# Optimization experiments

Hardware: AMD Instinct MI355X
Metric: run time of the kernel (lower is better)

The kernel has to match this reference:

```python
import jax, jax.numpy as jnp
import numpy as np

N_ENT = 50000
N_REL = 500
DIM = 128
B = 1024
N_EDGES = 800000
BN_EPS = 1e-5


def setup_inputs() -> dict:
    key = jax.random.key(0)
    ks = jax.random.split(key, 12)
    return {
        "E_emb": jax.random.normal(ks[0], (N_ENT, DIM), jnp.float32),
        "R_emb": jax.random.normal(ks[1], (N_REL, DIM), jnp.float32),
        "W1": jax.random.normal(ks[2], (DIM, DIM), jnp.float32) / np.sqrt(DIM),
        "b1": jax.random.normal(ks[3], (DIM,), jnp.float32) * 0.01,
        "W2": jax.random.normal(ks[4], (DIM, DIM), jnp.float32) / np.sqrt(DIM),
        "b2": jax.random.normal(ks[5], (DIM,), jnp.float32) * 0.01,
        "W": jax.random.normal(ks[6], (DIM, DIM), jnp.float32) / np.sqrt(DIM),
        "adj_vals": jax.random.uniform(ks[7], (N_EDGES,), jnp.float32) / 16.0,
        "bn0_gamma": jnp.ones((DIM,), jnp.float32),
        "bn0_beta": jnp.zeros((DIM,), jnp.float32),
        "bn1_gamma": jnp.ones((DIM,), jnp.float32),
        "bn1_beta": jnp.zeros((DIM,), jnp.float32),
        "batch_head": jax.random.randint(ks[8], (B,), 0, N_ENT, jnp.int32),
        "batch_rel": jax.random.randint(ks[9], (B,), 0, N_REL, jnp.int32),
        "init_ind": jnp.arange(N_ENT, dtype=jnp.int32),
        "adj_rows": jax.random.randint(ks[10], (N_EDGES,), 0, N_ENT, jnp.int32),
        "adj_cols": jax.random.randint(ks[11], (N_EDGES,), 0, N_ENT, jnp.int32),
    }


def _bn_eval(x, gamma, beta):
    # BatchNorm1d in eval mode with running_mean=0, running_var=1
    return x * (gamma / jnp.sqrt(1.0 + BN_EPS)) + beta


def _spmm(rows, cols, vals, dense):
    # out[i] = sum_{e: rows[e]==i} vals[e] * dense[cols[e]]
    gathered = dense[cols] * vals[:, None]  # [E, DIM]
    return jax.ops.segment_sum(gathered, rows, num_segments=N_ENT)


def reference(E_emb, R_emb, W1, b1, W2, b2, W, adj_vals,
              bn0_gamma, bn0_beta, bn1_gamma, bn1_beta,
              batch_head, batch_rel, init_ind, adj_rows, adj_cols):
    init_emb = E_emb[init_ind]                                  # [N, D]
    h = jax.nn.relu(_spmm(adj_rows, adj_cols, adj_vals, init_emb @ W1) + b1)
    h = jax.nn.relu(_spmm(adj_rows, adj_cols, adj_vals, h @ W2) + b2)
    final_emb = init_emb + h                                    # shortcut connection
    x = _bn_eval(final_emb[batch_head], bn0_gamma, bn0_beta)    # [B, D]
    r = R_emb[batch_rel]                                        # [B, D]
    W_mat = r @ W                                               # mat_vec_mul: [B, D]
    vm = _bn_eval(x * W_mat, bn1_gamma, bn1_beta)               # [B, D]
    dot = vm @ final_emb.T                                      # [B, N]
    return jax.nn.sigmoid(dot)
```

## Files before the change

kernel.cpp:

```cpp
#include <hip/hip_runtime.h>

#define N_ENT   50000
#define N_EDGES 800000
#define DIM     128
#define BATCH   1024

typedef _Float16 half_t;
typedef __attribute__((ext_vector_type(8))) _Float16 half8;
typedef __attribute__((ext_vector_type(2))) _Float16 half2v;
typedef __attribute__((ext_vector_type(4))) float float4v;
typedef __attribute__((ext_vector_type(2))) float float2v;

__global__ void k_hist(const int* __restrict__ rows, int* __restrict__ deg){
    int e = blockIdx.x*256 + threadIdx.x;
    if(e < N_EDGES) atomicAdd(&deg[rows[e]], 1);
}

__global__ void k_scan(const int* __restrict__ deg, int* __restrict__ row_start){
    __shared__ int part[1024];
    const int CH = 49;
    int t = threadIdx.x;
    int base = t*CH;
    int s = 0;
    for(int i=0;i<CH;i++){ int idx=base+i; if(idx<N_ENT) s += deg[idx]; }
    part[t]=s; __syncthreads();
    for(int off=1; off<1024; off<<=1){
        int v = part[t];
        int add = (t>=off)? part[t-off] : 0;
        __syncthreads();
        part[t] = v+add;
        __syncthreads();
    }
    int run = part[t]-s;
    for(int i=0;i<CH;i++){
        int idx=base+i;
        if(idx<=N_ENT){
            row_start[idx]=run;
            if(idx<N_ENT) run += deg[idx];
        }
    }
}

__global__ void k_scatter(const int* __restrict__ rows, const int* __restrict__ cols,
                          const float* __restrict__ vals, const int* __restrict__ row_start,
                          int* __restrict__ cursor, int* __restrict__ csr_col,
                          float* __restrict__ csr_val){
    int e = blockIdx.x*256 + threadIdx.x;
    if(e >= N_EDGES) return;
    int r = rows[e];
    int pos = row_start[r] + atomicAdd(&cursor[r], 1);
    csr_col[pos] = cols[e];
    csr_val[pos] = vals[e];
}

__global__ void k_prep(const float* __restrict__ W1, const float* __restrict__ W2,
                       half_t* __restrict__ W1T_hi, half_t* __restrict__ W1T_lo,
                       half_t* __restrict__ W2T_hi, half_t* __restrict__ W2T_lo){
    int i = blockIdx.x*256 + threadIdx.x;
    const float* src = (i < 16384) ? W1 : W2;
    half_t* dh = (i < 16384) ? W1T_hi : W2T_hi;
    half_t* dl = (i < 16384) ? W1T_lo : W2T_lo;
    int j = i & 16383;
    int d = j >> 7, c = j & 127;
    float f = src[j];
    half_t h = (half_t)f;
    dh[c*DIM + d] = h;
    dl[c*DIM + d] = (half_t)(f - (float)h);
}

__global__ __launch_bounds__(256) void k_mm1(const float* __restrict__ E,
                                             const int* __restrict__ init_ind,
                                             const half_t* __restrict__ WT_hi,
                                             const half_t* __restrict__ WT_lo,
                                             half_t* __restrict__ t_out){
    int wave = threadIdx.x >> 6, lane = threadIdx.x & 63;
    int mt = blockIdx.x*4 + wave;
    if(mt >= 3125) return;
    int m = lane & 15, q = lane >> 4;
    int row = init_ind[mt*16 + m];
    const float* ap = E + (long)row*DIM + q*8;
    float4v acc[8];
    #pragma unroll
    for(int i=0;i<8;i++) acc[i] = (float4v){0.f,0.f,0.f,0.f};
    #pragma unroll
    for(int ks=0; ks<4; ks++){
        float4v u0 = *(const float4v*)(ap + ks*32);
        float4v u1 = *(const float4v*)(ap + ks*32 + 4);
        half8 ah, al;
        #pragma unroll
        for(int j=0;j<8;j++){
            float fv = (j<4) ? u0[j] : u1[j-4];
            half_t h = (half_t)fv;
            ah[j] = h;
            al[j] = (half_t)(fv - (float)h);
        }
        #pragma unroll
        for(int nt=0; nt<8; nt++){
            half8 bh = *(const half8*)(WT_hi + (nt*16 + m)*DIM + ks*32 + q*8);
            half8 bl = *(const half8*)(WT_lo + (nt*16 + m)*DIM + ks*32 + q*8);
            acc[nt] = __builtin_amdgcn_mfma_f32_16x16x32_f16(ah, bh, acc[nt], 0,0,0);
            acc[nt] = __builtin_amdgcn_mfma_f32_16x16x32_f16(ah, bl, acc[nt], 0,0,0);
            acc[nt] = __builtin_amdgcn_mfma_f32_16x16x32_f16(al, bh, acc[nt], 0,0,0);
        }
    }
    #pragma unroll
    for(int nt=0; nt<8; nt++)
        #pragma unroll
        for(int r=0;r<4;r++)
            t_out[(mt*16 + q*4 + r)*DIM + nt*16 + m] = (half_t)acc[nt][r];
}

__global__ __launch_bounds__(256) void k_mm2(const half_t* __restrict__ h_hi,
                                             const half_t* __restrict__ h_lo,
                                             const half_t* __restrict__ WT_hi,
                                             const half_t* __restrict__ WT_lo,
                                             half_t* __restrict__ t_out){
    int wave = threadIdx.x >> 6, lane = threadIdx.x & 63;
    int mt = blockIdx.x*4 + wave;
    if(mt >= 3125) return;
    int m = lane & 15, q = lane >> 4;
    int row = mt*16 + m;
    const half_t* ah_p = h_hi + (long)row*DIM + q*8;
    const half_t* al_p = h_lo + (long)row*DIM + q*8;
    float4v acc[8];
    #pragma unroll
    for(int i=0;i<8;i++) acc[i] = (float4v){0.f,0.f,0.f,0.f};
    #pragma unroll
    for(int ks=0; ks<4; ks++){
        half8 ah = *(const half8*)(ah_p + ks*32);
        half8 al = *(const half8*)(al_p + ks*32);
        #pragma unroll
        for(int nt=0; nt<8; nt++){
            half8 bh = *(const half8*)(WT_hi + (nt*16 + m)*DIM + ks*32 + q*8);
            half8 bl = *(const half8*)(WT_lo + (nt*16 + m)*DIM + ks*32 + q*8);
            acc[nt] = __builtin_amdgcn_mfma_f32_16x16x32_f16(ah, bh, acc[nt], 0,0,0);
            acc[nt] = __builtin_amdgcn_mfma_f32_16x16x32_f16(ah, bl, acc[nt], 0,0,0);
            acc[nt] = __builtin_amdgcn_mfma_f32_16x16x32_f16(al, bh, acc[nt], 0,0,0);
        }
    }
    #pragma unroll
    for(int nt=0; nt<8; nt++)
        #pragma unroll
        for(int r=0;r<4;r++)
            t_out[(mt*16 + q*4 + r)*DIM + nt*16 + m] = (half_t)acc[nt][r];
}

__global__ __launch_bounds__(256) void k_spmm1(const half_t* __restrict__ t,
        const int* __restrict__ row_start, const int* __restrict__ csr_col,
        const float* __restrict__ csr_val, const float* __restrict__ b1,
        half_t* __restrict__ h_hi, half_t* __restrict__ h_lo){
    int wave = threadIdx.x>>6, lane = threadIdx.x&63;
    int i = blockIdx.x*4 + wave;
    if(i >= N_ENT) return;
    int e0 = __builtin_amdgcn_readfirstlane(row_start[i]);
    int e1 = __builtin_amdgcn_readfirstlane(row_start[i+1]);
    const half2v* tp = (const half2v*)t;
    float a0=0.f, a1=0.f;
    int e = e0;
    for(; e+4<=e1; e+=4){
        int c0=csr_col[e], c1=csr_col[e+1], c2=csr_col[e+2], c3=csr_col[e+3];
        float v0=csr_val[e], v1=csr_val[e+1], v2=csr_val[e+2], v3=csr_val[e+3];
        half2v p0=tp[c0*64+lane], p1=tp[c1*64+lane], p2=tp[c2*64+lane], p3=tp[c3*64+lane];
        a0 += v0*(float)p0[0]; a1 += v0*(float)p0[1];
        a0 += v1*(float)p1[0]; a1 += v1*(float)p1[1];
        a0 += v2*(float)p2[0]; a1 += v2*(float)p2[1];
        a0 += v3*(float)p3[0]; a1 += v3*(float)p3[1];
    }
    for(; e<e1; e++){
        int c = csr_col[e]; float v = csr_val[e];
        half2v p = tp[c*64+lane];
        a0 += v*(float)p[0]; a1 += v*(float)p[1];
    }
    float2v bb = *(const float2v*)(b1 + lane*2);
    float r0 = fmaxf(a0 + bb[0], 0.f);
    float r1 = fmaxf(a1 + bb[1], 0.f);
    half_t h0=(half_t)r0, h1=(half_t)r1;
    half2v hi = {h0, h1};
    half2v lo = {(half_t)(r0-(float)h0), (half_t)(r1-(float)h1)};
    *(half2v*)(h_hi + (long)i*DIM + lane*2) = hi;
    *(half2v*)(h_lo + (long)i*DIM + lane*2) = lo;
}

__global__ __launch_bounds__(256) void k_spmm2(const half_t* __restrict__ t,
        const int* __restrict__ row_start, const int* __restrict__ csr_col,
        const float* __restrict__ csr_val, const float* __restrict__ b2_,
        const float* __restrict__ E, const int* __restrict__ init_ind,
        half_t* __restrict__ fe_hi, half_t* __restrict__ fe_lo){
    int wave = threadIdx.x>>6, lane = threadIdx.x&63;
    int i = blockIdx.x*4 + wave;
    if(i >= N_ENT) return;
    int e0 = __builtin_amdgcn_readfirstlane(row_start[i]);
    int e1 = __builtin_amdgcn_readfirstlane(row_start[i+1]);
    const half2v* tp = (const half2v*)t;
    float a0=0.f, a1=0.f;
    int e = e0;
    for(; e+4<=e1; e+=4){
        int c0=csr_col[e], c1=csr_col[e+1], c2=csr_col[e+2], c3=csr_col[e+3];
        float v0=csr_val[e], v1=csr_val[e+1], v2=csr_val[e+2], v3=csr_val[e+3];
        half2v p0=tp[c0*64+lane], p1=tp[c1*64+lane], p2=tp[c2*64+lane], p3=tp[c3*64+lane];
        a0 += v0*(float)p0[0]; a1 += v0*(float)p0[1];
        a0 += v1*(float)p1[0]; a1 += v1*(float)p1[1];
        a0 += v2*(float)p2[0]; a1 += v2*(float)p2[1];
        a0 += v3*(float)p3[0]; a1 += v3*(float)p3[1];
    }
    for(; e<e1; e++){
        int c = csr_col[e]; float v = csr_val[e];
        half2v p = tp[c*64+lane];
        a0 += v*(float)p[0]; a1 += v*(float)p[1];
    }
    int erow = init_ind[i];
    float2v ev = *(const float2v*)(E + (long)erow*DIM + lane*2);
    float2v bb = *(const float2v*)(b2_ + lane*2);
    float f0 = ev[0] + fmaxf(a0 + bb[0], 0.f);
    float f1 = ev[1] + fmaxf(a1 + bb[1], 0.f);
    half_t h0=(half_t)f0, h1=(half_t)f1;
    half2v hi = {h0, h1};
    half2v lo = {(half_t)(f0-(float)h0), (half_t)(f1-(float)h1)};
    *(half2v*)(fe_hi + (long)i*DIM + lane*2) = hi;
    *(half2v*)(fe_lo + (long)i*DIM + lane*2) = lo;
}

__global__ __launch_bounds__(128) void k_vm(const float* __restrict__ R_emb,
        const float* __restrict__ W, const int* __restrict__ head,
        const int* __restrict__ rel, const half_t* __restrict__ fe_hi,
        const half_t* __restrict__ fe_lo, const float* __restrict__ g0v,
        const float* __restrict__ be0, const float* __restrict__ g1v,
        const float* __restrict__ be1, half_t* __restrict__ vm_hi,
        half_t* __restrict__ vm_lo){
    int b = blockIdx.x; int j = threadIdx.x;
    __shared__ float rs[DIM];
    int rid = rel[b], hid = head[b];
    rs[j] = R_emb[rid*DIM + j];
    __syncthreads();
    float acc = 0.f;
    #pragma unroll 8
    for(int d=0; d<DIM; d++) acc += rs[d] * W[d*DIM + j];
    const float inv = rsqrtf(1.f + 1e-5f);
    float fe = (float)fe_hi[(long)hid*DIM+j] + (float)fe_lo[(long)hid*DIM+j];
    float x  = fe * (g0v[j] * inv) + be0[j];
    float vmv = (x * acc) * (g1v[j] * inv) + be1[j];
    half_t hi = (half_t)vmv;
    vm_hi[b*DIM+j] = hi;
    vm_lo[b*DIM+j] = (half_t)(vmv - (float)hi);
}

__global__ __launch_bounds__(256) void k_big(const half_t* __restrict__ vm_hi,
        const half_t* __restrict__ vm_lo, const half_t* __restrict__ fe_h,
        float* __restrict__ out){
    __shared__ float sl[16*260];
    int wave = threadIdx.x>>6, lane = threadIdx.x&63;
    int m = lane&15, q = lane>>4;
    int b0 = blockIdx.y * 64;
    int n0 = blockIdx.x * 256 + wave*64;
    float4v acc[4][4];
    #pragma unroll
    for(int a=0;a<4;a++)
        #pragma unroll
        for(int b=0;b<4;b++) acc[a][b] = (float4v){0.f,0.f,0.f,0.f};
    #pragma unroll
    for(int ks=0; ks<4; ks++){
        half8 B[4], Ah[4], Al[4];
        #pragma unroll
        for(int nt=0;nt<4;nt++){
            int nr = n0 + nt*16 + m;
            if(nr > N_ENT-1) nr = N_ENT-1;
            B[nt] = *(const half8*)(fe_h + (long)nr*DIM + ks*32 + q*8);
        }
        #pragma unroll
        for(int mt=0;mt<4;mt++){
            long ao = (long)(b0 + mt*16 + m)*DIM + ks*32 + q*8;
            Ah[mt] = *(const half8*)(vm_hi + ao);
            Al[mt] = *(const half8*)(vm_lo + ao);
        }
        #pragma unroll
        for(int mt=0;mt<4;mt++)
            #pragma unroll
            for(int nt=0;nt<4;nt++){
                acc[mt][nt] = __builtin_amdgcn_mfma_f32_16x16x32_f16(Ah[mt], B[nt], acc[mt][nt], 0,0,0);
                acc[mt][nt] = __builtin_amdgcn_mfma_f32_16x16x32_f16(Al[mt], B[nt], acc[mt][nt], 0,0,0);
            }
    }
    int gcol = blockIdx.x*256 + lane*4;
    #pragma unroll
    for(int mt=0; mt<4; mt++){
        if(mt) __syncthreads();
        #pragma unroll
        for(int nt=0;nt<4;nt++)
            #pragma unroll
            for(int r=0;r<4;r++){
                float d = acc[mt][nt][r];
                float s = __fdividef(1.f, 1.f + __expf(-d));
                sl[(q*4+r)*260 + wave*64 + nt*16 + m] = s;
            }
        __syncthreads();
        if(gcol < N_ENT){
            #pragma unroll
            for(int k=0;k<4;k++){
                int lr = wave*4 + k;
                float4v vv = *(const float4v*)&sl[lr*260 + lane*4];
                long off = (long)(b0 + mt*16 + lr)*N_ENT + gcol;
                __builtin_nontemporal_store(vv, (float4v*)(out + off));
            }
        }
    }
}

extern "C" void kernel_launch(void* const* d_in, const int* in_sizes, int n_in,
                              void* d_out, int out_size, void* d_ws, size_t ws_size,
                              hipStream_t stream) {
    const float* E     = (const float*)d_in[0];
    const float* R_emb = (const float*)d_in[1];
    const float* W1    = (const float*)d_in[2];
    const float* b1    = (const float*)d_in[3];
    const float* W2    = (const float*)d_in[4];
    const float* b2_   = (const float*)d_in[5];
    const float* W     = (const float*)d_in[6];
    const float* vals  = (const float*)d_in[7];
    const float* g0v   = (const float*)d_in[8];
    const float* be0   = (const float*)d_in[9];
    const float* g1v   = (const float*)d_in[10];
    const float* be1   = (const float*)d_in[11];
    const int* head    = (const int*)d_in[12];
    const int* rel     = (const int*)d_in[13];
    const int* init_ind= (const int*)d_in[14];
    const int* rows    = (const int*)d_in[15];
    const int* cols    = (const int*)d_in[16];
    float* out = (float*)d_out;

    char* w = (char*)d_ws;
    int*    deg       = (int*)   (w + 0);
    int*    cursor    = (int*)   (w + 200000);
    int*    row_start = (int*)   (w + 400000);
    int*    csr_col   = (int*)   (w + 600064);
    float*  csr_val   = (float*) (w + 3800064);
    half_t* W1T_hi    = (half_t*)(w + 7000064);
    half_t* W1T_lo    = (half_t*)(w + 7032832);
    half_t* W2T_hi    = (half_t*)(w + 7065600);
    half_t* W2T_lo    = (half_t*)(w + 7098368);
    half_t* t         = (half_t*)(w + 7131136);
    half_t* h_hi      = (half_t*)(w + 19931136);
    half_t* h_lo      = (half_t*)(w + 32731136);
    half_t* fe_hi     = (half_t*)(w + 45531136);
    half_t* fe_lo     = (half_t*)(w + 58331136);
    half_t* vm_hi     = (half_t*)(w + 71131136);
    half_t* vm_lo     = (half_t*)(w + 71393280);

    hipMemsetAsync(deg, 0, 2*N_ENT*sizeof(int), stream);
    k_hist    <<<3125, 256, 0, stream>>>(rows, deg);
    k_scan    <<<1, 1024, 0, stream>>>(deg, row_start);
    k_scatter <<<3125, 256, 0, stream>>>(rows, cols, vals, row_start, cursor, csr_col, csr_val);
    k_prep    <<<128, 256, 0, stream>>>(W1, W2, W1T_hi, W1T_lo, W2T_hi, W2T_lo);
    k_mm1     <<<782, 256, 0, stream>>>(E, init_ind, W1T_hi, W1T_lo, t);
    k_spmm1   <<<12500, 256, 0, stream>>>(t, row_start, csr_col, csr_val, b1, h_hi, h_lo);
    k_mm2     <<<782, 256, 0, stream>>>(h_hi, h_lo, W2T_hi, W2T_lo, t);
    k_spmm2   <<<12500, 256, 0, stream>>>(t, row_start, csr_col, csr_val, b2_, E, init_ind, fe_hi, fe_lo);
    k_vm      <<<BATCH, 128, 0, stream>>>(R_emb, W, head, rel, fe_hi, fe_lo, g0v, be0, g1v, be1, vm_hi, vm_lo);
    k_big     <<<dim3(196, 16), 256, 0, stream>>>(vm_hi, vm_lo, fe_hi, out);
}
```

Measured before the change: 634.8 us.

## Fuse preprocessing kernels, fuse spmm1 with mm2, interleave CSR col/val pairs

Combines the histogram, weight transpose/split and the relation-times-W projection into one launch, and runs the scan alongside the first dense GEMM in a single launch. The first SpMM now writes its 16-row tile into shared memory and immediately multiplies it by W2, so the h_hi/h_lo intermediates no longer go through global memory. CSR columns and values are stored as interleaved int pairs, and the gather loops are unrolled to 8 edges. This removes launches and intermediate traffic. In exchange the fused SpMM-GEMM has fewer waves per row tile and a barrier before the MFMA stage, and the combined scan block may serialize behind the GEMM blocks.

```diff
diff --git a/kernel.cpp b/kernel.cpp
--- a/kernel.cpp
+++ b/kernel.cpp
@@ -1,6 +1,7 @@
 #include <hip/hip_runtime.h>
 
 #define N_ENT   50000
+#define N_REL   500
 #define N_EDGES 800000
 #define DIM     128
 #define BATCH   1024
@@ -10,71 +11,77 @@
 typedef __attribute__((ext_vector_type(2))) _Float16 half2v;
 typedef __attribute__((ext_vector_type(4))) float float4v;
 typedef __attribute__((ext_vector_type(2))) float float2v;
-
-__global__ void k_hist(const int* __restrict__ rows, int* __restrict__ deg){
-    int e = blockIdx.x*256 + threadIdx.x;
-    if(e < N_EDGES) atomicAdd(&deg[rows[e]], 1);
-}
-
-__global__ void k_scan(const int* __restrict__ deg, int* __restrict__ row_start){
-    __shared__ int part[1024];
-    const int CH = 49;
-    int t = threadIdx.x;
-    int base = t*CH;
-    int s = 0;
-    for(int i=0;i<CH;i++){ int idx=base+i; if(idx<N_ENT) s += deg[idx]; }
-    part[t]=s; __syncthreads();
-    for(int off=1; off<1024; off<<=1){
-        int v = part[t];
-        int add = (t>=off)? part[t-off] : 0;
+typedef __attribute__((ext_vector_type(2))) int int2v;
+
+__global__ __launch_bounds__(256) void k_pre(
+        const int* __restrict__ rows, int* __restrict__ deg,
+        const float* __restrict__ W1, const float* __restrict__ W2,
+        half_t* __restrict__ W1T_hi, half_t* __restrict__ W1T_lo,
+        half_t* __restrict__ W2T_hi, half_t* __restrict__ W2T_lo,
+        const float* __restrict__ R_emb, const float* __restrict__ W,
+        const int* __restrict__ rel, float* __restrict__ Wr){
+    int blk = blockIdx.x;
+    if(blk < 3125){
+        int e = blk*256 + threadIdx.x;
+        if(e < N_EDGES) atomicAdd(&deg[rows[e]], 1);
+    } else if(blk < 3253){
+        int i = (blk-3125)*256 + threadIdx.x;
+        const float* src = (i < 16384) ? W1 : W2;
+        half_t* dh = (i < 16384) ? W1T_hi : W2T_hi;
+        half_t* dl = (i < 16384) ? W1T_lo : W2T_lo;
+        int j = i & 16383;
+        int d = j >> 7, c = j & 127;
+        float f = src[j];
+        half_t h = (half_t)f;
+        dh[c*DIM + d] = h;
+        dl[c*DIM + d] = (half_t)(f - (float)h);
+    } else {
+        __shared__ float rs[2][DIM];
+        int half_id = threadIdx.x >> 7;
+        int bb = (blk-3253)*2 + half_id;
+        int j = threadIdx.x & 127;
+        int rid = rel[bb];
+        rs[half_id][j] = R_emb[rid*DIM + j];
         __syncthreads();
-        part[t] = v+add;
-        __syncthreads();
-    }
-    int run = part[t]-s;
-    for(int i=0;i<CH;i++){
-        int idx=base+i;
-        if(idx<=N_ENT){
-            row_start[idx]=run;
-            if(idx<N_ENT) run += deg[idx];
-        }
-    }
-}
-
-__global__ void k_scatter(const int* __restrict__ rows, const int* __restrict__ cols,
-                          const float* __restrict__ vals, const int* __restrict__ row_start,
-                          int* __restrict__ cursor, int* __restrict__ csr_col,
-                          float* __restrict__ csr_val){
-    int e = blockIdx.x*256 + threadIdx.x;
-    if(e >= N_EDGES) return;
-    int r = rows[e];
-    int pos = row_start[r] + atomicAdd(&cursor[r], 1);
-    csr_col[pos] = cols[e];
-    csr_val[pos] = vals[e];
-}
-
-__global__ void k_prep(const float* __restrict__ W1, const float* __restrict__ W2,
-                       half_t* __restrict__ W1T_hi, half_t* __restrict__ W1T_lo,
-                       half_t* __restrict__ W2T_hi, half_t* __restrict__ W2T_lo){
-    int i = blockIdx.x*256 + threadIdx.x;
-    const float* src = (i < 16384) ? W1 : W2;
-    half_t* dh = (i < 16384) ? W1T_hi : W2T_hi;
-    half_t* dl = (i < 16384) ? W1T_lo : W2T_lo;
-    int j = i & 16383;
-    int d = j >> 7, c = j & 127;
-    float f = src[j];
-    half_t h = (half_t)f;
-    dh[c*DIM + d] = h;
-    dl[c*DIM + d] = (half_t)(f - (float)h);
-}
-
-__global__ __launch_bounds__(256) void k_mm1(const float* __restrict__ E,
-                                             const int* __restrict__ init_ind,
-                                             const half_t* __restrict__ WT_hi,
-                                             const half_t* __restrict__ WT_lo,
-                                             half_t* __restrict__ t_out){
+        float acc = 0.f;
+        #pragma unroll 8
+        for(int d=0; d<DIM; d++) acc += rs[half_id][d] * W[d*DIM + j];
+        Wr[bb*DIM + j] = acc;
+    }
+}
+
+__global__ __launch_bounds__(1024) void k_scan_mm1(
+        const int* __restrict__ deg, int* __restrict__ row_start,
+        const float* __restrict__ E, const int* __restrict__ init_ind,
+        const half_t* __restrict__ WT_hi, const half_t* __restrict__ WT_lo,
+        half_t* __restrict__ t_out){
+    if(blockIdx.x == 0){
+        __shared__ int part[1024];
+        const int CH = 49;
+        int t = threadIdx.x;
+        int base = t*CH;
+        int s = 0;
+        for(int i=0;i<CH;i++){ int idx=base+i; if(idx<N_ENT) s += deg[idx]; }
+        part[t]=s; __syncthreads();
+        for(int off=1; off<1024; off<<=1){
+            int v = part[t];
+            int add = (t>=off)? part[t-off] : 0;
+            __syncthreads();
+            part[t] = v+add;
+            __syncthreads();
+        }
+        int run = part[t]-s;
+        for(int i=0;i<CH;i++){
+            int idx=base+i;
+            if(idx<=N_ENT){
+                row_start[idx]=run;
+                if(idx<N_ENT) run += deg[idx];
+            }
+        }
+        return;
+    }
     int wave = threadIdx.x >> 6, lane = threadIdx.x & 63;
-    int mt = blockIdx.x*4 + wave;
+    int mt = (blockIdx.x-1)*16 + wave;
     if(mt >= 3125) return;
     int m = lane & 15, q = lane >> 4;
     int row = init_ind[mt*16 + m];
@@ -110,81 +117,107 @@
             t_out[(mt*16 + q*4 + r)*DIM + nt*16 + m] = (half_t)acc[nt][r];
 }
 
-__global__ __launch_bounds__(256) void k_mm2(const half_t* __restrict__ h_hi,
-                                             const half_t* __restrict__ h_lo,
-                                             const half_t* __restrict__ WT_hi,
-                                             const half_t* __restrict__ WT_lo,
-                                             half_t* __restrict__ t_out){
-    int wave = threadIdx.x >> 6, lane = threadIdx.x & 63;
-    int mt = blockIdx.x*4 + wave;
-    if(mt >= 3125) return;
+__global__ __launch_bounds__(256) void k_scatter(const int* __restrict__ rows,
+        const int* __restrict__ cols, const float* __restrict__ vals,
+        const int* __restrict__ row_start, int* __restrict__ cursor,
+        int2v* __restrict__ csr){
+    int e = blockIdx.x*256 + threadIdx.x;
+    if(e >= N_EDGES) return;
+    int r = rows[e];
+    int pos = row_start[r] + atomicAdd(&cursor[r], 1);
+    int2v p;
+    p[0] = cols[e];
+    p[1] = __float_as_int(vals[e]);
+    csr[pos] = p;
+}
+
+__global__ __launch_bounds__(256) void k_sp1mm2(
+        const half_t* __restrict__ t, const int* __restrict__ row_start,
+        const int2v* __restrict__ csr, const float* __restrict__ b1,
+        const half_t* __restrict__ WT_hi, const half_t* __restrict__ WT_lo,
+        half_t* __restrict__ t2){
+    __shared__ half_t hh[16][136];
+    __shared__ half_t hl[16][136];
+    int wave = threadIdx.x>>6, lane = threadIdx.x&63;
+    int mt = blockIdx.x;
+    const half2v* tp = (const half2v*)t;
+    float2v bb = *(const float2v*)(b1 + lane*2);
+    for(int rr=0; rr<4; rr++){
+        int i = mt*16 + wave*4 + rr;
+        int e0 = __builtin_amdgcn_readfirstlane(row_start[i]);
+        int e1 = __builtin_amdgcn_readfirstlane(row_start[i+1]);
+        float a0=0.f, a1=0.f;
+        int e = e0;
+        for(; e+8<=e1; e+=8){
+            int2v p0=csr[e],   p1=csr[e+1], p2=csr[e+2], p3=csr[e+3];
+            int2v p4=csr[e+4], p5=csr[e+5], p6=csr[e+6], p7=csr[e+7];
+            half2v g0=tp[p0[0]*64+lane], g1=tp[p1[0]*64+lane], g2=tp[p2[0]*64+lane], g3=tp[p3[0]*64+lane];
+            half2v g4=tp[p4[0]*64+lane], g5=tp[p5[0]*64+lane], g6=tp[p6[0]*64+lane], g7=tp[p7[0]*64+lane];
+            float v0=__int_as_float(p0[1]), v1=__int_as_float(p1[1]), v2=__int_as_float(p2[1]), v3=__int_as_float(p3[1]);
+            float v4=__int_as_float(p4[1]), v5=__int_as_float(p5[1]), v6=__int_as_float(p6[1]), v7=__int_as_float(p7[1]);
+            a0 += v0*(float)g0[0]; a1 += v0*(float)g0[1];
+            a0 += v1*(float)g1[0]; a1 += v1*(float)g1[1];
+            a0 += v2*(float)g2[0]; a1 += v2*(float)g2[1];
+            a0 += v3*(float)g3[0]; a1 += v3*(float)g3[1];
+            a0 += v4*(float)g4[0]; a1 += v4*(float)g4[1];
+            a0 += v5*(float)g5[0]; a1 += v5*(float)g5[1];
+            a0 += v6*(float)g6[0]; a1 += v6*(float)g6[1];
+            a0 += v7*(float)g7[0]; a1 += v7*(float)g7[1];
+        }
+        for(; e+4<=e1; e+=4){
+            int2v p0=csr[e], p1=csr[e+1], p2=csr[e+2], p3=csr[e+3];
+            half2v g0=tp[p0[0]*64+lane], g1=tp[p1[0]*64+lane], g2=tp[p2[0]*64+lane], g3=tp[p3[0]*64+lane];
+            float v0=__int_as_float(p0[1]), v1=__int_as_float(p1[1]), v2=__int_as_float(p2[1]), v3=__int_as_float(p3[1]);
+            a0 += v0*(float)g0[0]; a1 += v0*(float)g0[1];
+            a0 += v1*(float)g1[0]; a1 += v1*(float)g1[1];
+            a0 += v2*(float)g2[0]; a1 += v2*(float)g2[1];
+            a0 += v3*(float)g3[0]; a1 += v3*(float)g3[1];
+        }
+        for(; e<e1; e++){
+            int2v p = csr[e];
+            half2v g = tp[p[0]*64+lane];
+            float v = __int_as_float(p[1]);
+            a0 += v*(float)g[0]; a1 += v*(float)g[1];
+        }
+        float r0 = fmaxf(a0 + bb[0], 0.f);
+        float r1 = fmaxf(a1 + bb[1], 0.f);
+        half_t h0=(half_t)r0, h1=(half_t)r1;
+        int row = wave*4 + rr;
+        *(half2v*)&hh[row][lane*2] = (half2v){h0, h1};
+        *(half2v*)&hl[row][lane*2] = (half2v){(half_t)(r0-(float)h0), (half_t)(r1-(float)h1)};
+    }
+    __syncthreads();
     int m = lane & 15, q = lane >> 4;
-    int row = mt*16 + m;
-    const half_t* ah_p = h_hi + (long)row*DIM + q*8;
-    const half_t* al_p = h_lo + (long)row*DIM + q*8;
-    float4v acc[8];
-    #pragma unroll
-    for(int i=0;i<8;i++) acc[i] = (float4v){0.f,0.f,0.f,0.f};
+    float4v acc[2];
+    acc[0] = (float4v){0.f,0.f,0.f,0.f};
+    acc[1] = (float4v){0.f,0.f,0.f,0.f};
     #pragma unroll
     for(int ks=0; ks<4; ks++){
-        half8 ah = *(const half8*)(ah_p + ks*32);
-        half8 al = *(const half8*)(al_p + ks*32);
-        #pragma unroll
-        for(int nt=0; nt<8; nt++){
+        half8 ah = *(const half8*)&hh[m][ks*32 + q*8];
+        half8 al = *(const half8*)&hl[m][ks*32 + q*8];
+        #pragma unroll
+        for(int n=0; n<2; n++){
+            int nt = wave*2 + n;
             half8 bh = *(const half8*)(WT_hi + (nt*16 + m)*DIM + ks*32 + q*8);
             half8 bl = *(const half8*)(WT_lo + (nt*16 + m)*DIM + ks*32 + q*8);
-            acc[nt] = __builtin_amdgcn_mfma_f32_16x16x32_f16(ah, bh, acc[nt], 0,0,0);
-            acc[nt] = __builtin_amdgcn_mfma_f32_16x16x32_f16(ah, bl, acc[nt], 0,0,0);
-            acc[nt] = __builtin_amdgcn_mfma_f32_16x16x32_f16(al, bh, acc[nt], 0,0,0);
-        }
-    }
-    #pragma unroll
-    for(int nt=0; nt<8; nt++)
+            acc[n] = __builtin_amdgcn_mfma_f32_16x16x32_f16(ah, bh, acc[n], 0,0,0);
+            acc[n] = __builtin_amdgcn_mfma_f32_16x16x32_f16(ah, bl, acc[n], 0,0,0);
+            acc[n] = __builtin_amdgcn_mfma_f32_16x16x32_f16(al, bh, acc[n], 0,0,0);
+        }
+    }
+    #pragma unroll
+    for(int n=0; n<2; n++){
+        int nt = wave*2 + n;
         #pragma unroll
         for(int r=0;r<4;r++)
-            t_out[(mt*16 + q*4 + r)*DIM + nt*16 + m] = (half_t)acc[nt][r];
-}
-
-__global__ __launch_bounds__(256) void k_spmm1(const half_t* __restrict__ t,
-        const int* __restrict__ row_start, const int* __restrict__ csr_col,
-        const float* __restrict__ csr_val, const float* __restrict__ b1,
-        half_t* __restrict__ h_hi, half_t* __restrict__ h_lo){
-    int wave = threadIdx.x>>6, lane = threadIdx.x&63;
-    int i = blockIdx.x*4 + wave;
-    if(i >= N_ENT) return;
-    int e0 = __builtin_amdgcn_readfirstlane(row_start[i]);
-    int e1 = __builtin_amdgcn_readfirstlane(row_start[i+1]);
-    const half2v* tp = (const half2v*)t;
-    float a0=0.f, a1=0.f;
-    int e = e0;
-    for(; e+4<=e1; e+=4){
-        int c0=csr_col[e], c1=csr_col[e+1], c2=csr_col[e+2], c3=csr_col[e+3];
-        float v0=csr_val[e], v1=csr_val[e+1], v2=csr_val[e+2], v3=csr_val[e+3];
-        half2v p0=tp[c0*64+lane], p1=tp[c1*64+lane], p2=tp[c2*64+lane], p3=tp[c3*64+lane];
-        a0 += v0*(float)p0[0]; a1 += v0*(float)p0[1];
-        a0 += v1*(float)p1[0]; a1 += v1*(float)p1[1];
-        a0 += v2*(float)p2[0]; a1 += v2*(float)p2[1];
-        a0 += v3*(float)p3[0]; a1 += v3*(float)p3[1];
-    }
-    for(; e<e1; e++){
-        int c = csr_col[e]; float v = csr_val[e];
-        half2v p = tp[c*64+lane];
-        a0 += v*(float)p[0]; a1 += v*(float)p[1];
-    }
-    float2v bb = *(const float2v*)(b1 + lane*2);
-    float r0 = fmaxf(a0 + bb[0], 0.f);
-    float r1 = fmaxf(a1 + bb[1], 0.f);
-    half_t h0=(half_t)r0, h1=(half_t)r1;
-    half2v hi = {h0, h1};
-    half2v lo = {(half_t)(r0-(float)h0), (half_t)(r1-(float)h1)};
-    *(half2v*)(h_hi + (long)i*DIM + lane*2) = hi;
-    *(half2v*)(h_lo + (long)i*DIM + lane*2) = lo;
+            t2[(mt*16 + q*4 + r)*DIM + nt*16 + m] = (half_t)acc[n][r];
+    }
 }
 
 __global__ __launch_bounds__(256) void k_spmm2(const half_t* __restrict__ t,
-        const int* __restrict__ row_start, const int* __restrict__ csr_col,
-        const float* __restrict__ csr_val, const float* __restrict__ b2_,
-        const float* __restrict__ E, const int* __restrict__ init_ind,
+        const int* __restrict__ row_start, const int2v* __restrict__ csr,
+        const float* __restrict__ b2_, const float* __restrict__ E,
+        const int* __restrict__ init_ind,
         half_t* __restrict__ fe_hi, half_t* __restrict__ fe_lo){
     int wave = threadIdx.x>>6, lane = threadIdx.x&63;
     int i = blockIdx.x*4 + wave;
@@ -194,19 +227,36 @@
     const half2v* tp = (const half2v*)t;
     float a0=0.f, a1=0.f;
     int e = e0;
+    for(; e+8<=e1; e+=8){
+        int2v p0=csr[e],   p1=csr[e+1], p2=csr[e+2], p3=csr[e+3];
+        int2v p4=csr[e+4], p5=csr[e+5], p6=csr[e+6], p7=csr[e+7];
+        half2v g0=tp[p0[0]*64+lane], g1=tp[p1[0]*64+lane], g2=tp[p2[0]*64+lane], g3=tp[p3[0]*64+lane];
+        half2v g4=tp[p4[0]*64+lane], g5=tp[p5[0]*64+lane], g6=tp[p6[0]*64+lane], g7=tp[p7[0]*64+lane];
+        float v0=__int_as_float(p0[1]), v1=__int_as_float(p1[1]), v2=__int_as_float(p2[1]), v3=__int_as_float(p3[1]);
+        float v4=__int_as_float(p4[1]), v5=__int_as_float(p5[1]), v6=__int_as_float(p6[1]), v7=__int_as_float(p7[1]);
+        a0 += v0*(float)g0[0]; a1 += v0*(float)g0[1];
+        a0 += v1*(float)g1[0]; a1 += v1*(float)g1[1];
+        a0 += v2*(float)g2[0]; a1 += v2*(float)g2[1];
+        a0 += v3*(float)g3[0]; a1 += v3*(float)g3[1];
+        a0 += v4*(float)g4[0]; a1 += v4*(float)g4[1];
+        a0 += v5*(float)g5[0]; a1 += v5*(float)g5[1];
+        a0 += v6*(float)g6[0]; a1 += v6*(float)g6[1];
+        a0 += v7*(float)g7[0]; a1 += v7*(float)g7[1];
+    }
     for(; e+4<=e1; e+=4){
-        int c0=csr_col[e], c1=csr_col[e+1], c2=csr_col[e+2], c3=csr_col[e+3];
-        float v0=csr_val[e], v1=csr_val[e+1], v2=csr_val[e+2], v3=csr_val[e+3];
-        half2v p0=tp[c0*64+lane], p1=tp[c1*64+lane], p2=tp[c2*64+lane], p3=tp[c3*64+lane];
-        a0 += v0*(float)p0[0]; a1 += v0*(float)p0[1];
-        a0 += v1*(float)p1[0]; a1 += v1*(float)p1[1];
-        a0 += v2*(float)p2[0]; a1 += v2*(float)p2[1];
-        a0 += v3*(float)p3[0]; a1 += v3*(float)p3[1];
+        int2v p0=csr[e], p1=csr[e+1], p2=csr[e+2], p3=csr[e+3];
+        half2v g0=tp[p0[0]*64+lane], g1=tp[p1[0]*64+lane], g2=tp[p2[0]*64+lane], g3=tp[p3[0]*64+lane];
+        float v0=__int_as_float(p0[1]), v1=__int_as_float(p1[1]), v2=__int_as_float(p2[1]), v3=__int_as_float(p3[1]);
+        a0 += v0*(float)g0[0]; a1 += v0*(float)g0[1];
+        a0 += v1*(float)g1[0]; a1 += v1*(float)g1[1];
+        a0 += v2*(float)g2[0]; a1 += v2*(float)g2[1];
+        a0 += v3*(float)g3[0]; a1 += v3*(float)g3[1];
     }
     for(; e<e1; e++){
-        int c = csr_col[e]; float v = csr_val[e];
-        half2v p = tp[c*64+lane];
-        a0 += v*(float)p[0]; a1 += v*(float)p[1];
+        int2v p = csr[e];
+        half2v g = tp[p[0]*64+lane];
+        float v = __int_as_float(p[1]);
+        a0 += v*(float)g[0]; a1 += v*(float)g[1];
     }
     int erow = init_ind[i];
     float2v ev = *(const float2v*)(E + (long)erow*DIM + lane*2);
@@ -220,28 +270,22 @@
     *(half2v*)(fe_lo + (long)i*DIM + lane*2) = lo;
 }
 
-__global__ __launch_bounds__(128) void k_vm(const float* __restrict__ R_emb,
-        const float* __restrict__ W, const int* __restrict__ head,
-        const int* __restrict__ rel, const half_t* __restrict__ fe_hi,
+__global__ __launch_bounds__(256) void k_vm(const float* __restrict__ Wr,
+        const int* __restrict__ head, const half_t* __restrict__ fe_hi,
         const half_t* __restrict__ fe_lo, const float* __restrict__ g0v,
         const float* __restrict__ be0, const float* __restrict__ g1v,
         const float* __restrict__ be1, half_t* __restrict__ vm_hi,
         half_t* __restrict__ vm_lo){
-    int b = blockIdx.x; int j = threadIdx.x;
-    __shared__ float rs[DIM];
-    int rid = rel[b], hid = head[b];
-    rs[j] = R_emb[rid*DIM + j];
-    __syncthreads();
-    float acc = 0.f;
-    #pragma unroll 8
-    for(int d=0; d<DIM; d++) acc += rs[d] * W[d*DIM + j];
+    int idx = blockIdx.x*256 + threadIdx.x;
+    int b = idx >> 7, j = idx & 127;
+    int hid = head[b];
     const float inv = rsqrtf(1.f + 1e-5f);
     float fe = (float)fe_hi[(long)hid*DIM+j] + (float)fe_lo[(long)hid*DIM+j];
     float x  = fe * (g0v[j] * inv) + be0[j];
-    float vmv = (x * acc) * (g1v[j] * inv) + be1[j];
+    float vmv = (x * Wr[idx]) * (g1v[j] * inv) + be1[j];
     half_t hi = (half_t)vmv;
-    vm_hi[b*DIM+j] = hi;
-    vm_lo[b*DIM+j] = (half_t)(vmv - (float)hi);
+    vm_hi[idx] = hi;
+    vm_lo[idx] = (half_t)(vmv - (float)hi);
 }
 
 __global__ __launch_bounds__(256) void k_big(const half_t* __restrict__ vm_hi,
@@ -331,29 +375,26 @@
     int*    deg       = (int*)   (w + 0);
     int*    cursor    = (int*)   (w + 200000);
     int*    row_start = (int*)   (w + 400000);
-    int*    csr_col   = (int*)   (w + 600064);
-    float*  csr_val   = (float*) (w + 3800064);
+    int2v*  csr       = (int2v*) (w + 600064);
     half_t* W1T_hi    = (half_t*)(w + 7000064);
     half_t* W1T_lo    = (half_t*)(w + 7032832);
     half_t* W2T_hi    = (half_t*)(w + 7065600);
     half_t* W2T_lo    = (half_t*)(w + 7098368);
-    half_t* t         = (half_t*)(w + 7131136);
-    half_t* h_hi      = (half_t*)(w + 19931136);
-    half_t* h_lo      = (half_t*)(w + 32731136);
-    half_t* fe_hi     = (half_t*)(w + 45531136);
-    half_t* fe_lo     = (half_t*)(w + 58331136);
-    half_t* vm_hi     = (half_t*)(w + 71131136);
-    half_t* vm_lo     = (half_t*)(w + 71393280);
+    float*  Wr        = (float*) (w + 7131136);
+    half_t* t         = (half_t*)(w + 7655424);
+    half_t* t2        = (half_t*)(w + 20455424);
+    half_t* fe_hi     = (half_t*)(w + 33255424);
+    half_t* fe_lo     = (half_t*)(w + 46055424);
+    half_t* vm_hi     = (half_t*)(w + 58855424);
+    half_t* vm_lo     = (half_t*)(w + 59117568);
 
     hipMemsetAsync(deg, 0, 2*N_ENT*sizeof(int), stream);
-    k_hist    <<<3125, 256, 0, stream>>>(rows, deg);
-    k_scan    <<<1, 1024, 0, stream>>>(deg, row_start);
-    k_scatter <<<3125, 256, 0, stream>>>(rows, cols, vals, row_start, cursor, csr_col, csr_val);
-    k_prep    <<<128, 256, 0, stream>>>(W1, W2, W1T_hi, W1T_lo, W2T_hi, W2T_lo);
-    k_mm1     <<<782, 256, 0, stream>>>(E, init_ind, W1T_hi, W1T_lo, t);
-    k_spmm1   <<<12500, 256, 0, stream>>>(t, row_start, csr_col, csr_val, b1, h_hi, h_lo);
-    k_mm2     <<<782, 256, 0, stream>>>(h_hi, h_lo, W2T_hi, W2T_lo, t);
-    k_spmm2   <<<12500, 256, 0, stream>>>(t, row_start, csr_col, csr_val, b2_, E, init_ind, fe_hi, fe_lo);
-    k_vm      <<<BATCH, 128, 0, stream>>>(R_emb, W, head, rel, fe_hi, fe_lo, g0v, be0, g1v, be1, vm_hi, vm_lo);
-    k_big     <<<dim3(196, 16), 256, 0, stream>>>(vm_hi, vm_lo, fe_hi, out);
-}
+    k_pre      <<<3765, 256, 0, stream>>>(rows, deg, W1, W2, W1T_hi, W1T_lo, W2T_hi, W2T_lo,
+                                          R_emb, W, rel, Wr);
+    k_scan_mm1 <<<197, 1024, 0, stream>>>(deg, row_start, E, init_ind, W1T_hi, W1T_lo, t);
+    k_scatter  <<<3125, 256, 0, stream>>>(rows, cols, vals, row_start, cursor, csr);
+    k_sp1mm2   <<<3125, 256, 0, stream>>>(t, row_start, csr, b1, W2T_hi, W2T_lo, t2);
+    k_spmm2    <<<12500, 256, 0, stream>>>(t2, row_start, csr, b2_, E, init_ind, fe_hi, fe_lo);
+    k_vm       <<<512, 256, 0, stream>>>(Wr, head, fe_hi, fe_lo, g0v, be0, g1v, be1, vm_hi, vm_lo);
+    k_big      <<<dim3(196, 16), 256, 0, stream>>>(vm_hi, vm_lo, fe_hi, out);
+}
```

Measured after the change: 560.1 us. 1.13x faster.
